# Performance work log

Measured on AMD Instinct MI355X. Metric: run time of the kernel, lower is better.

## Reference

```python
import jax, jax.numpy as jnp
import numpy as np

BLOCK_M = 64          # Triton BLOCK_M assumed from first autotune config
SPEAKER, SCENE, STAGE = 1, 2, 3
NUM_HEADS, HEAD_SIZE = 12, 64


def setup_inputs() -> dict:
    key = jax.random.key(0)
    ks = jax.random.split(key, 6)
    B, T, E = 4, 1024, 768
    H, D = NUM_HEADS, HEAD_SIZE
    x = jax.random.normal(ks[0], (B, T, E), jnp.float32)
    idx = jax.random.randint(ks[1], (B, T), 0, 32000)
    struct_embed = jax.random.normal(ks[2], (4, E), jnp.float32) * 0.02
    w_qkv = jax.random.normal(ks[3], (3 * H * D, E), jnp.float32) * 0.02
    w_out = jax.random.normal(ks[4], (E, H * D), jnp.float32) * 0.02
    b_out = jnp.zeros((E,), jnp.float32)
    return {"x": x, "idx": idx, "struct_embed": struct_embed,
            "w_qkv": w_qkv, "w_out": w_out, "b_out": b_out}


def _attention(q, k, v):
    # q,k,v: [B,H,T,D]. Faithful to the Triton kernel (eval mode):
    # q/k rounded to bf16, fp32 dot, logit clamp [-30,30], exp clamp 1e5,
    # +1e-10 denom, output rounded to bf16. Query rows with
    # (row % BLOCK_M) % 3 == 0 are zeroed by the kernel's load mask.
    T, D = q.shape[2], q.shape[3]
    keep = ((jnp.arange(T) % BLOCK_M) % 3 != 0).astype(q.dtype)
    qb = q.astype(jnp.bfloat16).astype(jnp.float32) * keep[None, None, :, None]
    kb = k.astype(jnp.bfloat16).astype(jnp.float32)
    scale = 1.0 / np.sqrt(D).astype(np.float32)
    scores = jnp.einsum('bhmd,bhnd->bhmn', qb, kb) * scale
    scores = jnp.clip(scores, -30.0, 30.0)
    m = jnp.max(scores, axis=-1, keepdims=True)
    p = jnp.minimum(jnp.exp(scores - m), 1e5)
    acc = jnp.einsum('bhmn,bhnd->bhmd', p, v)
    out = acc / (jnp.sum(p, axis=-1, keepdims=True) + 1e-10)
    return out.astype(jnp.bfloat16).astype(jnp.float32)


def reference(x, idx, struct_embed, w_qkv, w_out, b_out):
    B, T, E = x.shape
    H, D = NUM_HEADS, HEAD_SIZE
    # structure embedding addition (struct_dropout is identity in eval)
    struct_ids = ((idx == SPEAKER) * 1 + (idx == SCENE) * 2
                  + (idx == STAGE) * 3)
    x = x + struct_embed[struct_ids]
    # fused QKV projection (no bias)
    qkv = x @ w_qkv.T                              # [B,T,3HD]
    q, k, v = jnp.split(qkv, 3, axis=-1)
    q = q.reshape(B, T, H, D).transpose(0, 2, 1, 3)
    k = k.reshape(B, T, H, D).transpose(0, 2, 1, 3)
    v = v.reshape(B, T, H, D).transpose(0, 2, 1, 3)
    attn = _attention(q, k, v)                     # [B,H,T,D]
    attn = attn.transpose(0, 2, 1, 3).reshape(B, T, H * D)
    return attn @ w_out.T + b_out
```

## Files before the change

kernel.cpp:

```cpp
#include <hip/hip_runtime.h>
#include <hip/hip_bf16.h>

typedef __attribute__((ext_vector_type(8))) short bf16x8;
typedef __attribute__((ext_vector_type(4))) short bf16x4;
typedef __attribute__((ext_vector_type(4))) float f32x4;

#define MFMA16(a, b, c) __builtin_amdgcn_mfma_f32_16x16x32_bf16(a, b, c, 0, 0, 0)
#define VMCNT4() asm volatile("s_waitcnt vmcnt(4)" ::: "memory")
#define VMCNT0() asm volatile("s_waitcnt vmcnt(0)" ::: "memory")

__device__ __forceinline__ unsigned short f2bf(float f) {
  unsigned u = __float_as_uint(f);
  u += 0x7fff + ((u >> 16) & 1);
  return (unsigned short)(u >> 16);
}
__device__ __forceinline__ float bf2f(unsigned short s) {
  return __uint_as_float(((unsigned)s) << 16);
}
__device__ __forceinline__ void gload16(const unsigned short* g, unsigned short* l) {
  __builtin_amdgcn_global_load_lds((const __attribute__((address_space(1))) void*)g,
                                   (__attribute__((address_space(3))) void*)l, 16, 0, 0);
}
__device__ __forceinline__ int xcd_swz(int lin, int nwg) {
  int cpx = nwg >> 3;
  return (lin & 7) * cpx + (lin >> 3);
}

__global__ __launch_bounds__(256) void prep_all(const float* __restrict__ x,
                                                const int* __restrict__ idx,
                                                const float* __restrict__ se,
                                                const float* __restrict__ wqkv,
                                                const float* __restrict__ wout,
                                                unsigned short* __restrict__ xb,
                                                unsigned short* __restrict__ wqkvb,
                                                unsigned short* __restrict__ woutb) {
  int bid = blockIdx.x;
  int tid = threadIdx.x;
  if (bid < 3072) {
    int i = bid * 256 + tid;
    int row = i / 192, c4 = i % 192;
    int id = idx[row];
    int sid = (id == 1) ? 1 : (id == 2) ? 2 : (id == 3) ? 3 : 0;
    float4 v = ((const float4*)x)[i];
    float4 s = ((const float4*)se)[sid * 192 + c4];
    ushort4 o;
    o.x = f2bf(v.x + s.x); o.y = f2bf(v.y + s.y);
    o.z = f2bf(v.z + s.z); o.w = f2bf(v.w + s.w);
    *(ushort4*)(xb + (size_t)i * 4) = o;
  } else if (bid < 3072 + 1728) {
    int i = (bid - 3072) * 256 + tid;
    float4 v = ((const float4*)wqkv)[i];
    ushort4 u;
    u.x = f2bf(v.x); u.y = f2bf(v.y); u.z = f2bf(v.z); u.w = f2bf(v.w);
    ((ushort4*)wqkvb)[i] = u;
  } else {
    int i = (bid - 4800) * 256 + tid;
    float4 v = ((const float4*)wout)[i];
    ushort4 u;
    u.x = f2bf(v.x); u.y = f2bf(v.y); u.z = f2bf(v.z); u.w = f2bf(v.w);
    ((ushort4*)woutb)[i] = u;
  }
}

__global__ __launch_bounds__(256) void gemm_qkv(const unsigned short* __restrict__ A,
                                                const unsigned short* __restrict__ B,
                                                unsigned short* __restrict__ Cout,
                                                unsigned short* __restrict__ vT,
                                                int N, int K) {
  __shared__ unsigned short As[2][4096];
  __shared__ unsigned short Bs[2][4096];
  int tid = threadIdx.x;
  int lane = tid & 63, wid = tid >> 6;
  int l15 = lane & 15, lhi = lane >> 4;
  int wr = wid >> 1, wc = wid & 1;
  int gy = gridDim.y;
  int lin = blockIdx.x + gridDim.x * blockIdx.y;
  int swz = xcd_swz(lin, gridDim.x * gy);
  long tm = (long)(swz / gy) * 128;
  long tn = (long)(swz % gy) * 128;
  f32x4 acc[4][4];
  const f32x4 z4 = {0.f, 0.f, 0.f, 0.f};
  for (int i = 0; i < 4; ++i)
    for (int j = 0; j < 4; ++j) acc[i][j] = z4;

  int wbase = tid & ~63;
  int row0 = tid >> 2;
  int kc = (tid & 3) * 8;
  const unsigned short* Ar0 = &A[(tm + row0) * (long)K + kc];
  const unsigned short* Ar1 = &A[(tm + 64 + row0) * (long)K + kc];
  const unsigned short* Br0 = &B[(tn + row0) * (long)K + kc];
  const unsigned short* Br1 = &B[(tn + 64 + row0) * (long)K + kc];

  auto stage = [&](int b, int k0) {
    gload16(Ar0 + k0, &As[b][wbase * 8]);
    gload16(Ar1 + k0, &As[b][2048 + wbase * 8]);
    gload16(Br0 + k0, &Bs[b][wbase * 8]);
    gload16(Br1 + k0, &Bs[b][2048 + wbase * 8]);
  };

  stage(0, 0);
  __syncthreads();
  int buf = 0;
  for (int k0 = 0; k0 < K; k0 += 32) {
    if (k0 + 32 < K) stage(buf ^ 1, k0 + 32);
    bf16x8 af[4], bfr[4];
#pragma unroll
    for (int mi = 0; mi < 4; ++mi)
      af[mi] = *(const bf16x8*)&As[buf][(wr * 64 + mi * 16 + l15) * 32 + lhi * 8];
#pragma unroll
    for (int nj = 0; nj < 4; ++nj)
      bfr[nj] = *(const bf16x8*)&Bs[buf][(wc * 64 + nj * 16 + l15) * 32 + lhi * 8];
#pragma unroll
    for (int mi = 0; mi < 4; ++mi)
#pragma unroll
      for (int nj = 0; nj < 4; ++nj)
        acc[mi][nj] = MFMA16(af[mi], bfr[nj], acc[mi][nj]);
    __syncthreads();
    buf ^= 1;
  }

  if (tn >= 1536) {
    int b = (int)(tm >> 10);
    int hbase = (int)((tn - 1536) >> 6) + wc;
    int tb = (int)(tm & 1023) + wr * 64 + lhi * 4;
#pragma unroll
    for (int nj = 0; nj < 4; ++nj) {
      int dd = nj * 16 + l15;
      size_t vbase = ((size_t)(b * 12 + hbase)) * 65536 + (size_t)dd * 1024;
#pragma unroll
      for (int mi = 0; mi < 4; ++mi) {
        ushort4 o;
        o.x = f2bf(acc[mi][nj][0]); o.y = f2bf(acc[mi][nj][1]);
        o.z = f2bf(acc[mi][nj][2]); o.w = f2bf(acc[mi][nj][3]);
        *(ushort4*)&vT[vbase + tb + mi * 16] = o;
      }
    }
    return;
  }

#pragma unroll
  for (int mi = 0; mi < 4; ++mi) {
    long row = tm + wr * 64 + mi * 16 + lhi * 4;
#pragma unroll
    for (int nj = 0; nj < 4; ++nj) {
      long col = tn + wc * 64 + nj * 16 + l15;
#pragma unroll
      for (int r = 0; r < 4; ++r)
        Cout[(row + r) * (long)N + col] = f2bf(acc[mi][nj][r]);
    }
  }
}

__global__ __launch_bounds__(256) void gemm_out(const unsigned short* __restrict__ A,
                                                const unsigned short* __restrict__ B,
                                                float* __restrict__ Cout,
                                                const float* __restrict__ bias,
                                                int N, int K) {
  __shared__ unsigned short As[2][64 * 32];
  __shared__ unsigned short Bs[2][64 * 32];
  int tid = threadIdx.x;
  int lane = tid & 63, w = tid >> 6;
  int l15 = lane & 15, lhi = lane >> 4;
  int gy = gridDim.y;
  int lin = blockIdx.x + gridDim.x * blockIdx.y;
  int swz = xcd_swz(lin, gridDim.x * gy);
  long tm = (long)(swz / gy) * 64;
  long tn = (long)(swz % gy) * 64;
  f32x4 acc[4];
  const f32x4 z4 = {0.f, 0.f, 0.f, 0.f};
#pragma unroll
  for (int n = 0; n < 4; ++n) acc[n] = z4;

  int wbase8 = (tid & ~63) * 8;
  int row0 = tid >> 2;
  int kc = (tid & 3) * 8;
  const unsigned short* Ar = &A[(tm + row0) * (long)K + kc];
  const unsigned short* Br = &B[(tn + row0) * (long)K + kc];

  auto stage = [&](int b, int k0) {
    gload16(Ar + k0, &As[b][wbase8]);
    gload16(Br + k0, &Bs[b][wbase8]);
  };

  stage(0, 0);
  __syncthreads();
  int buf = 0;
  for (int k0 = 0; k0 < K; k0 += 32) {
    if (k0 + 32 < K) stage(buf ^ 1, k0 + 32);
    bf16x8 af = *(const bf16x8*)&As[buf][(w * 16 + l15) * 32 + lhi * 8];
    bf16x8 bfr[4];
#pragma unroll
    for (int n = 0; n < 4; ++n)
      bfr[n] = *(const bf16x8*)&Bs[buf][(n * 16 + l15) * 32 + lhi * 8];
#pragma unroll
    for (int n = 0; n < 4; ++n)
      acc[n] = MFMA16(af, bfr[n], acc[n]);
    __syncthreads();
    buf ^= 1;
  }

  long row = tm + w * 16 + lhi * 4;
#pragma unroll
  for (int n = 0; n < 4; ++n) {
    long col = tn + n * 16 + l15;
    float bv = bias[col];
#pragma unroll
    for (int r = 0; r < 4; ++r)
      Cout[(row + r) * (long)N + col] = acc[n][r] + bv;
  }
}

__global__ __launch_bounds__(256) void attn_fwd(const unsigned short* __restrict__ qkv,
                                                const unsigned short* __restrict__ vT,
                                                unsigned short* __restrict__ attnb) {
  __shared__ unsigned short Ks[3][4096];
  __shared__ unsigned short Vs[3][4096];
  int tid = threadIdx.x;
  int lane = tid & 63, w = tid >> 6;
  int l15 = lane & 15, lhi = lane >> 4;
  int sw = l15 & 7;
  int lin = blockIdx.x + gridDim.x * blockIdx.y;
  int swz = xcd_swz(lin, 768);
  int qt = swz & 15, bh = swz >> 4;
  int b = bh / 12, h = bh % 12;

  int qrl = w * 16 + l15;
  bf16x8 qf0 = {0, 0, 0, 0, 0, 0, 0, 0}, qf1 = {0, 0, 0, 0, 0, 0, 0, 0};
  if (qrl % 3 != 0) {
    const unsigned short* qp =
        &qkv[(size_t)(b * 1024 + qt * 64 + qrl) * 2304 + h * 64 + lhi * 8];
    qf0 = *(const bf16x8*)qp;
    qf1 = *(const bf16x8*)(qp + 32);
  }

  int r8 = lane >> 3;
  int cK = ((lane & 7) ^ r8) << 3;
  int wbase = (tid & ~63) * 8;
  const unsigned short* kg = qkv + (size_t)(b * 1024) * 2304 + 768 + h * 64 + cK;
  const unsigned short* vg = vT + (size_t)bh * 65536 + cK;

  auto stage = [&](int bufi, int t) {
    size_t k0 = (size_t)t * 64;
#pragma unroll
    for (int p = 0; p < 2; ++p) {
      int row = p * 32 + w * 8 + r8;
      gload16(kg + (k0 + row) * 2304, &Ks[bufi][p * 2048 + wbase]);
      gload16(vg + (size_t)row * 1024 + k0, &Vs[bufi][p * 2048 + wbase]);
    }
  };

  stage(0, 0);
  stage(1, 1);

  const f32x4 z4 = {0.f, 0.f, 0.f, 0.f};
  f32x4 acc[4];
#pragma unroll
  for (int dg = 0; dg < 4; ++dg) acc[dg] = z4;
  f32x4 accd = z4;
  const short one_bf = (short)0x3F80;
  const bf16x8 ONES = {one_bf, one_bf, one_bf, one_bf, one_bf, one_bf, one_bf, one_bf};

  int bc = 0, bp = 2;
  for (int t = 0; t < 16; ++t) {
    if (t < 15) VMCNT4(); else VMCNT0();
    __builtin_amdgcn_s_barrier();
    if (t + 2 < 16) stage(bp, t + 2);
    const unsigned short* ks = Ks[bc];
    const unsigned short* vs = Vs[bc];

    bf16x8 paf[2];
#pragma unroll
    for (int g = 0; g < 4; ++g) {
      const unsigned short* kr = &ks[(g * 16 + l15) * 64];
      bf16x8 kf0 = *(const bf16x8*)&kr[(lhi ^ sw) << 3];
      bf16x8 kf1 = *(const bf16x8*)&kr[((lhi + 4) ^ sw) << 3];
      f32x4 sg = MFMA16(kf0, qf0, z4);
      sg = MFMA16(kf1, qf1, sg);
#pragma unroll
      for (int r = 0; r < 4; ++r) {
        float pv = exp2f(sg[r] * 0.18033688011f);
        paf[g >> 1][(g & 1) * 4 + r] = (short)f2bf(pv);
      }
    }

    __builtin_amdgcn_s_setprio(1);
    accd = MFMA16(paf[0], ONES, accd);
    accd = MFMA16(paf[1], ONES, accd);
#pragma unroll
    for (int dg = 0; dg < 4; ++dg) {
      const unsigned short* vr = &vs[(dg * 16 + l15) * 64];
#pragma unroll
      for (int kh = 0; kh < 2; ++kh) {
        int o0 = kh * 32 + lhi * 4;
        int o1 = o0 + 16;
        bf16x4 v0 = *(const bf16x4*)&vr[(((o0 >> 3) ^ sw) << 3) + (o0 & 7)];
        bf16x4 v1 = *(const bf16x4*)&vr[(((o1 >> 3) ^ sw) << 3) + (o1 & 7)];
        bf16x8 vf = __builtin_shufflevector(v0, v1, 0, 1, 2, 3, 4, 5, 6, 7);
        acc[dg] = MFMA16(paf[kh], vf, acc[dg]);
      }
    }
    __builtin_amdgcn_s_setprio(0);
    bc = (bc == 2) ? 0 : bc + 1;
    bp = (bp == 2) ? 0 : bp + 1;
  }

#pragma unroll
  for (int r = 0; r < 4; ++r) {
    float inv = 1.f / (accd[r] + 1e-10f);
    int orow = qt * 64 + w * 16 + lhi * 4 + r;
    size_t obase = (size_t)(b * 1024 + orow) * 768 + h * 64;
#pragma unroll
    for (int dg = 0; dg < 4; ++dg)
      attnb[obase + dg * 16 + l15] = f2bf(acc[dg][r] * inv);
  }
}

extern "C" void kernel_launch(void* const* d_in, const int* in_sizes, int n_in,
                              void* d_out, int out_size, void* d_ws, size_t ws_size,
                              hipStream_t stream) {
  (void)in_sizes; (void)n_in; (void)out_size; (void)ws_size;
  const float* x    = (const float*)d_in[0];
  const int*   idx  = (const int*)d_in[1];
  const float* se   = (const float*)d_in[2];
  const float* wqkv = (const float*)d_in[3];
  const float* wout = (const float*)d_in[4];
  const float* bout = (const float*)d_in[5];
  float* out = (float*)d_out;

  char* ws = (char*)d_ws;
  unsigned short* xb    = (unsigned short*)(ws);
  unsigned short* wqkvb = (unsigned short*)(ws + 6291456);
  unsigned short* woutb = (unsigned short*)(ws + 9830400);
  unsigned short* qkvb  = (unsigned short*)(ws + 11010048);
  unsigned short* vT    = (unsigned short*)(ws + 29884416);
  unsigned short* attnb = (unsigned short*)(ws + 36175872);

  prep_all<<<5376, 256, 0, stream>>>(x, idx, se, wqkv, wout, xb, wqkvb, woutb);
  gemm_qkv<<<dim3(32, 18), 256, 0, stream>>>(xb, wqkvb, qkvb, vT, 2304, 768);
  attn_fwd<<<dim3(16, 48), 256, 0, stream>>>(qkvb, vT, attnb);
  gemm_out<<<dim3(64, 12), 256, 0, stream>>>(attnb, woutb, out, bout, 768, 768);
}
```

Before: 86.31 us.

## Permute V-transpose token layout so attention loads V with single 16-byte LDS reads

The QKV GEMM epilogue now writes transposed V with a permuted token order inside each 64-token group, so each lane's eight P·V operand values are contiguous. The attention kernel can then read each V fragment with one 16-byte LDS load instead of two 8-byte loads plus a shuffle. It also hoists all K and V fragment loads ahead of the MFMA and exp work to expose more load latency hiding. The trade-off is higher register pressure from holding sixteen fragments at once, and correctness depends on the producer permutation matching the consumer's lane mapping exactly.

```diff
diff --git a/kernel.cpp b/kernel.cpp
--- a/kernel.cpp
+++ b/kernel.cpp
@@ -2,7 +2,6 @@
 #include <hip/hip_bf16.h>
 
 typedef __attribute__((ext_vector_type(8))) short bf16x8;
-typedef __attribute__((ext_vector_type(4))) short bf16x4;
 typedef __attribute__((ext_vector_type(4))) float f32x4;
 
 #define MFMA16(a, b, c) __builtin_amdgcn_mfma_f32_16x16x32_bf16(a, b, c, 0, 0, 0)
@@ -122,7 +121,7 @@
   if (tn >= 1536) {
     int b = (int)(tm >> 10);
     int hbase = (int)((tn - 1536) >> 6) + wc;
-    int tb = (int)(tm & 1023) + wr * 64 + lhi * 4;
+    int tmw = (int)(tm & 1023) + wr * 64;
 #pragma unroll
     for (int nj = 0; nj < 4; ++nj) {
       int dd = nj * 16 + l15;
@@ -132,7 +131,7 @@
         ushort4 o;
         o.x = f2bf(acc[mi][nj][0]); o.y = f2bf(acc[mi][nj][1]);
         o.z = f2bf(acc[mi][nj][2]); o.w = f2bf(acc[mi][nj][3]);
-        *(ushort4*)&vT[vbase + tb + mi * 16] = o;
+        *(ushort4*)&vT[vbase + tmw + (mi >> 1) * 32 + lhi * 8 + (mi & 1) * 4] = o;
       }
     }
     return;
@@ -268,14 +267,27 @@
     const unsigned short* ks = Ks[bc];
     const unsigned short* vs = Vs[bc];
 
-    bf16x8 paf[2];
+    bf16x8 kf[4][2];
 #pragma unroll
     for (int g = 0; g < 4; ++g) {
       const unsigned short* kr = &ks[(g * 16 + l15) * 64];
-      bf16x8 kf0 = *(const bf16x8*)&kr[(lhi ^ sw) << 3];
-      bf16x8 kf1 = *(const bf16x8*)&kr[((lhi + 4) ^ sw) << 3];
-      f32x4 sg = MFMA16(kf0, qf0, z4);
-      sg = MFMA16(kf1, qf1, sg);
+      kf[g][0] = *(const bf16x8*)&kr[(lhi ^ sw) << 3];
+      kf[g][1] = *(const bf16x8*)&kr[((lhi + 4) ^ sw) << 3];
+    }
+    bf16x8 vfr[4][2];
+#pragma unroll
+    for (int dg = 0; dg < 4; ++dg) {
+      const unsigned short* vr = &vs[(dg * 16 + l15) * 64];
+#pragma unroll
+      for (int kh = 0; kh < 2; ++kh)
+        vfr[dg][kh] = *(const bf16x8*)&vr[((kh * 4 + lhi) ^ sw) << 3];
+    }
+
+    bf16x8 paf[2];
+#pragma unroll
+    for (int g = 0; g < 4; ++g) {
+      f32x4 sg = MFMA16(kf[g][0], qf0, z4);
+      sg = MFMA16(kf[g][1], qf1, sg);
 #pragma unroll
       for (int r = 0; r < 4; ++r) {
         float pv = exp2f(sg[r] * 0.18033688011f);
@@ -287,18 +299,10 @@
     accd = MFMA16(paf[0], ONES, accd);
     accd = MFMA16(paf[1], ONES, accd);
 #pragma unroll
-    for (int dg = 0; dg < 4; ++dg) {
-      const unsigned short* vr = &vs[(dg * 16 + l15) * 64];
-#pragma unroll
-      for (int kh = 0; kh < 2; ++kh) {
-        int o0 = kh * 32 + lhi * 4;
-        int o1 = o0 + 16;
-        bf16x4 v0 = *(const bf16x4*)&vr[(((o0 >> 3) ^ sw) << 3) + (o0 & 7)];
-        bf16x4 v1 = *(const bf16x4*)&vr[(((o1 >> 3) ^ sw) << 3) + (o1 & 7)];
-        bf16x8 vf = __builtin_shufflevector(v0, v1, 0, 1, 2, 3, 4, 5, 6, 7);
-        acc[dg] = MFMA16(paf[kh], vf, acc[dg]);
-      }
-    }
+    for (int dg = 0; dg < 4; ++dg)
+#pragma unroll
+      for (int kh = 0; kh < 2; ++kh)
+        acc[dg] = MFMA16(paf[kh], vfr[dg][kh], acc[dg]);
     __builtin_amdgcn_s_setprio(0);
     bc = (bc == 2) ? 0 : bc + 1;
     bp = (bp == 2) ? 0 : bp + 1;
```

Measured after the change: 82.54 us. 1.05x faster.

## Split attention key tiles across warps and reduce partial outputs via LDS atomics

Applied to the files above, without the earlier changes.

Each warp now handles all 64 query rows of the block against its own 16-key slice of every key tile, where before each warp owned 16 query rows and covered all keys. This cuts the per-warp K/V LDS fragment reads and lets the PV product use 16x16x16 MFMAs with K=16 matching the slice. The partial accumulators and denominators are then summed across warps through float atomics in shared memory before normalization. This adds fourfold accumulator registers, an LDS atomic reduction epilogue, and more QK MFMA work per warp.

```diff
diff --git a/kernel.cpp b/kernel.cpp
--- a/kernel.cpp
+++ b/kernel.cpp
@@ -8,14 +8,20 @@
 #define MFMA16(a, b, c) __builtin_amdgcn_mfma_f32_16x16x32_bf16(a, b, c, 0, 0, 0)
 #define VMCNT4() asm volatile("s_waitcnt vmcnt(4)" ::: "memory")
 #define VMCNT0() asm volatile("s_waitcnt vmcnt(0)" ::: "memory")
+
+__device__ __forceinline__ f32x4 mfma_k16(bf16x4 a, bf16x4 b, f32x4 c) {
+#if __has_builtin(__builtin_amdgcn_mfma_f32_16x16x16bf16_1k)
+  return __builtin_amdgcn_mfma_f32_16x16x16bf16_1k(a, b, c, 0, 0, 0);
+#else
+  asm volatile("v_mfma_f32_16x16x16_bf16 %0, %1, %2, %0" : "+v"(c) : "v"(a), "v"(b));
+  return c;
+#endif
+}
 
 __device__ __forceinline__ unsigned short f2bf(float f) {
   unsigned u = __float_as_uint(f);
   u += 0x7fff + ((u >> 16) & 1);
   return (unsigned short)(u >> 16);
-}
-__device__ __forceinline__ float bf2f(unsigned short s) {
-  return __uint_as_float(((unsigned)s) << 16);
 }
 __device__ __forceinline__ void gload16(const unsigned short* g, unsigned short* l) {
   __builtin_amdgcn_global_load_lds((const __attribute__((address_space(1))) void*)g,
@@ -213,8 +219,7 @@
 __global__ __launch_bounds__(256) void attn_fwd(const unsigned short* __restrict__ qkv,
                                                 const unsigned short* __restrict__ vT,
                                                 unsigned short* __restrict__ attnb) {
-  __shared__ unsigned short Ks[3][4096];
-  __shared__ unsigned short Vs[3][4096];
+  __shared__ __align__(16) unsigned short smem[24576];
   int tid = threadIdx.x;
   int lane = tid & 63, w = tid >> 6;
   int l15 = lane & 15, lhi = lane >> 4;
@@ -224,13 +229,18 @@
   int qt = swz & 15, bh = swz >> 4;
   int b = bh / 12, h = bh % 12;
 
-  int qrl = w * 16 + l15;
-  bf16x8 qf0 = {0, 0, 0, 0, 0, 0, 0, 0}, qf1 = {0, 0, 0, 0, 0, 0, 0, 0};
-  if (qrl % 3 != 0) {
-    const unsigned short* qp =
-        &qkv[(size_t)(b * 1024 + qt * 64 + qrl) * 2304 + h * 64 + lhi * 8];
-    qf0 = *(const bf16x8*)qp;
-    qf1 = *(const bf16x8*)(qp + 32);
+  bf16x8 qf[4][2];
+#pragma unroll
+  for (int qg = 0; qg < 4; ++qg) {
+    qf[qg][0] = bf16x8{0, 0, 0, 0, 0, 0, 0, 0};
+    qf[qg][1] = bf16x8{0, 0, 0, 0, 0, 0, 0, 0};
+    int qrl = qg * 16 + l15;
+    if (qrl % 3 != 0) {
+      const unsigned short* qp =
+          &qkv[(size_t)(b * 1024 + qt * 64 + qrl) * 2304 + h * 64 + lhi * 8];
+      qf[qg][0] = *(const bf16x8*)qp;
+      qf[qg][1] = *(const bf16x8*)(qp + 32);
+    }
   }
 
   int r8 = lane >> 3;
@@ -239,13 +249,15 @@
   const unsigned short* kg = qkv + (size_t)(b * 1024) * 2304 + 768 + h * 64 + cK;
   const unsigned short* vg = vT + (size_t)bh * 65536 + cK;
 
+  auto Ks = [&](int bi) { return smem + bi * 4096; };
+  auto Vs = [&](int bi) { return smem + 12288 + bi * 4096; };
   auto stage = [&](int bufi, int t) {
     size_t k0 = (size_t)t * 64;
 #pragma unroll
     for (int p = 0; p < 2; ++p) {
       int row = p * 32 + w * 8 + r8;
-      gload16(kg + (k0 + row) * 2304, &Ks[bufi][p * 2048 + wbase]);
-      gload16(vg + (size_t)row * 1024 + k0, &Vs[bufi][p * 2048 + wbase]);
+      gload16(kg + (k0 + row) * 2304, Ks(bufi) + p * 2048 + wbase);
+      gload16(vg + (size_t)row * 1024 + k0, Vs(bufi) + p * 2048 + wbase);
     }
   };
 
@@ -253,65 +265,87 @@
   stage(1, 1);
 
   const f32x4 z4 = {0.f, 0.f, 0.f, 0.f};
-  f32x4 acc[4];
-#pragma unroll
-  for (int dg = 0; dg < 4; ++dg) acc[dg] = z4;
-  f32x4 accd = z4;
+  f32x4 acc[4][4];
+#pragma unroll
+  for (int qg = 0; qg < 4; ++qg)
+#pragma unroll
+    for (int dg = 0; dg < 4; ++dg) acc[qg][dg] = z4;
+  f32x4 accd[4] = {z4, z4, z4, z4};
   const short one_bf = (short)0x3F80;
-  const bf16x8 ONES = {one_bf, one_bf, one_bf, one_bf, one_bf, one_bf, one_bf, one_bf};
+  const bf16x4 ONES4 = {one_bf, one_bf, one_bf, one_bf};
+
+  int koff0 = (lhi ^ sw) << 3, koff1 = ((lhi + 4) ^ sw) << 3;
+  int vch = ((w * 2 + (lhi >> 1)) ^ sw);
+  int voff = l15 * 64 + vch * 8 + (lhi & 1) * 4;
 
   int bc = 0, bp = 2;
   for (int t = 0; t < 16; ++t) {
     if (t < 15) VMCNT4(); else VMCNT0();
     __builtin_amdgcn_s_barrier();
     if (t + 2 < 16) stage(bp, t + 2);
-    const unsigned short* ks = Ks[bc];
-    const unsigned short* vs = Vs[bc];
-
-    bf16x8 paf[2];
-#pragma unroll
-    for (int g = 0; g < 4; ++g) {
-      const unsigned short* kr = &ks[(g * 16 + l15) * 64];
-      bf16x8 kf0 = *(const bf16x8*)&kr[(lhi ^ sw) << 3];
-      bf16x8 kf1 = *(const bf16x8*)&kr[((lhi + 4) ^ sw) << 3];
-      f32x4 sg = MFMA16(kf0, qf0, z4);
-      sg = MFMA16(kf1, qf1, sg);
+    const unsigned short* ks = Ks(bc);
+    const unsigned short* vs = Vs(bc);
+
+    const unsigned short* kr = &ks[(w * 16 + l15) * 64];
+    bf16x8 kf0 = *(const bf16x8*)&kr[koff0];
+    bf16x8 kf1 = *(const bf16x8*)&kr[koff1];
+    bf16x4 vfr4[4];
+#pragma unroll
+    for (int dg = 0; dg < 4; ++dg)
+      vfr4[dg] = *(const bf16x4*)&vs[dg * 1024 + voff];
+
+    bf16x4 paf4[4];
+#pragma unroll
+    for (int qg = 0; qg < 4; ++qg) {
+      f32x4 sg = MFMA16(kf0, qf[qg][0], z4);
+      sg = MFMA16(kf1, qf[qg][1], sg);
 #pragma unroll
       for (int r = 0; r < 4; ++r) {
         float pv = exp2f(sg[r] * 0.18033688011f);
-        paf[g >> 1][(g & 1) * 4 + r] = (short)f2bf(pv);
+        paf4[qg][r] = (short)f2bf(pv);
       }
     }
 
     __builtin_amdgcn_s_setprio(1);
-    accd = MFMA16(paf[0], ONES, accd);
-    accd = MFMA16(paf[1], ONES, accd);
-#pragma unroll
-    for (int dg = 0; dg < 4; ++dg) {
-      const unsigned short* vr = &vs[(dg * 16 + l15) * 64];
-#pragma unroll
-      for (int kh = 0; kh < 2; ++kh) {
-        int o0 = kh * 32 + lhi * 4;
-        int o1 = o0 + 16;
-        bf16x4 v0 = *(const bf16x4*)&vr[(((o0 >> 3) ^ sw) << 3) + (o0 & 7)];
-        bf16x4 v1 = *(const bf16x4*)&vr[(((o1 >> 3) ^ sw) << 3) + (o1 & 7)];
-        bf16x8 vf = __builtin_shufflevector(v0, v1, 0, 1, 2, 3, 4, 5, 6, 7);
-        acc[dg] = MFMA16(paf[kh], vf, acc[dg]);
-      }
-    }
+#pragma unroll
+    for (int qg = 0; qg < 4; ++qg)
+      accd[qg] = mfma_k16(paf4[qg], ONES4, accd[qg]);
+#pragma unroll
+    for (int dg = 0; dg < 4; ++dg)
+#pragma unroll
+      for (int qg = 0; qg < 4; ++qg)
+        acc[qg][dg] = mfma_k16(paf4[qg], vfr4[dg], acc[qg][dg]);
     __builtin_amdgcn_s_setprio(0);
     bc = (bc == 2) ? 0 : bc + 1;
     bp = (bp == 2) ? 0 : bp + 1;
   }
 
+  __syncthreads();
+  float* fb = (float*)smem;
+  for (int i = tid; i < 4160; i += 256) fb[i] = 0.f;
+  __syncthreads();
+#pragma unroll
+  for (int qg = 0; qg < 4; ++qg) {
+#pragma unroll
+    for (int dg = 0; dg < 4; ++dg)
+#pragma unroll
+      for (int r = 0; r < 4; ++r)
+        atomicAdd(&fb[(qg * 16 + lhi * 4 + r) * 64 + dg * 16 + l15], acc[qg][dg][r]);
+    if (l15 == 0)
+#pragma unroll
+      for (int r = 0; r < 4; ++r)
+        atomicAdd(&fb[4096 + qg * 16 + lhi * 4 + r], accd[qg][r]);
+  }
+  __syncthreads();
+
 #pragma unroll
   for (int r = 0; r < 4; ++r) {
-    float inv = 1.f / (accd[r] + 1e-10f);
-    int orow = qt * 64 + w * 16 + lhi * 4 + r;
-    size_t obase = (size_t)(b * 1024 + orow) * 768 + h * 64;
+    int q = w * 16 + lhi * 4 + r;
+    float inv = 1.f / (fb[4096 + q] + 1e-10f);
+    size_t obase = (size_t)(b * 1024 + qt * 64 + q) * 768 + h * 64;
 #pragma unroll
     for (int dg = 0; dg < 4; ++dg)
-      attnb[obase + dg * 16 + l15] = f2bf(acc[dg][r] * inv);
+      attnb[obase + dg * 16 + l15] = f2bf(fb[q * 64 + dg * 16 + l15] * inv);
   }
 }
 
```

Result: slower. 153.0 us (+77.3%).
